# Optimization experiments

Measured on AMD Instinct MI355X. Metric: run time of the kernel, lower is better.

Reference implementation:

```python
import jax, jax.numpy as jnp
import numpy as np

N = 8192
IN_F = 256
HID = 192
OUT_F = 3


def setup_inputs() -> dict:
    key = jax.random.key(0)
    ks = jax.random.split(key, 8)
    features = jax.random.normal(ks[0], (N, IN_F), dtype=jnp.float32)
    # dense (row-stochastic-ish) adjacency; sparse pattern scaled to keep magnitudes sane
    adj = (jax.random.uniform(ks[1], (N, N), dtype=jnp.float32) < (32.0 / N)).astype(jnp.float32) / 32.0
    def winit(k, shape):
        stdv = 0.6 * 6.0 / np.sqrt(shape[0] + shape[1])
        return jax.random.uniform(k, shape, jnp.float32, -stdv, stdv)
    W1 = winit(ks[2], (IN_F, HID))
    b1 = jax.random.uniform(ks[3], (HID,), jnp.float32, -0.1, 0.1)
    W_mid = jnp.stack([winit(jax.random.fold_in(ks[4], i), (HID, HID)) for i in range(12)])
    b_mid = jax.random.uniform(ks[5], (12, HID), jnp.float32, -0.1, 0.1)
    W_out = winit(ks[6], (HID, OUT_F))
    b_out = jax.random.uniform(ks[7], (OUT_F,), jnp.float32, -0.1, 0.1)
    return dict(features=features, adj=adj, W1=W1, b1=b1,
                W_mid=W_mid, b_mid=b_mid, W_out=W_out, b_out=b_out)


def zngcn(x, adj, W, b):
    # support = x @ W; first side_len cols aggregated over adj, rest passed through
    support = x @ W
    side_len = max(W.shape[1] // 3, 2)
    side_1 = adj @ support[:, :side_len]   # [N, side_len]
    out = jnp.concatenate([side_1, support[:, side_len:]], axis=1)
    return out + b


def reference(features, adj, W1, b1, W_mid, b_mid, W_out, b_out):
    relu = jax.nn.relu
    x = relu(zngcn(features, adj, W1, b1))            # gc1
    x = relu(zngcn(x, adj, W_mid[0], b_mid[0]))       # gc2
    feat = (features[:, :HID] + x) * 0.5
    # gc3..gc12 as 5 residual pairs (W_mid indices 1..10)
    for i in (1, 3, 5, 7, 9):
        x = relu(zngcn(feat, adj, W_mid[i], b_mid[i]))
        x = relu(zngcn(x, adj, W_mid[i + 1], b_mid[i + 1]))
        feat = (feat + x) * 0.5
    # gc13 single layer (W_mid index 11)
    x = relu(zngcn(feat, adj, W_mid[11], b_mid[11]))
    feat = (feat + x) * 0.5
    coords = zngcn(feat, adj, W_out, b_out)           # gc14
    return coords, feat
```

## Files before the change

kernel.cpp:

```cpp
#include <hip/hip_runtime.h>
#include <hip/hip_bf16.h>

#define N_NODES 8192
#define CAP 128
#define XSTR 200
#define FFSTR 193
#define NBLK 512
#define SUPSZ (N_NODES * 64)
#define LEAF_BASE 16384

typedef short s16x8 __attribute__((ext_vector_type(8)));
typedef float f32x4 __attribute__((ext_vector_type(4)));
typedef unsigned short u16x8 __attribute__((ext_vector_type(8)));

__device__ __forceinline__ void cstoref(float* p, float v) {
    __hip_atomic_store(p, v, __ATOMIC_RELAXED, __HIP_MEMORY_SCOPE_AGENT);
}
__device__ __forceinline__ void cstoreh(unsigned short* p, unsigned short v) {
    __hip_atomic_store(p, v, __ATOMIC_RELAXED, __HIP_MEMORY_SCOPE_AGENT);
}
__device__ __forceinline__ void cstorei(int* p, int v) {
    __hip_atomic_store(p, v, __ATOMIC_RELAXED, __HIP_MEMORY_SCOPE_AGENT);
}
__device__ __forceinline__ int cloadi(const int* p) {
    return __hip_atomic_load(p, __ATOMIC_RELAXED, __HIP_MEMORY_SCOPE_AGENT);
}
__device__ __forceinline__ float b2f(unsigned short u) {
    union { unsigned int i; float f; } c; c.i = ((unsigned int)u) << 16; return c.f;
}

__global__ __launch_bounds__(256) void prep(
    const unsigned int* __restrict__ adj,
    const float* __restrict__ W1, const float* __restrict__ Wm,
    int* __restrict__ cnt, int* __restrict__ cols,
    unsigned short* __restrict__ Wt1, unsigned short* __restrict__ WtM)
{
    const int tid = threadIdx.x;
    if (blockIdx.x >= 2048) {
        int idx = (int)(blockIdx.x - 2048) * 256 + tid;
        if (idx >= 6144 + 55296) return;
        const float* src; unsigned short* dst; int KT, t, c, lane;
        if (idx < 6144) {
            KT = 8; src = W1; dst = Wt1;
            t = idx / 512; c = (idx >> 6) & 7; lane = idx & 63;
        } else {
            int r = idx - 6144;
            int mat = r / 4608;
            int rem = r % 4608;
            KT = 6; src = Wm + (size_t)mat * 36864; dst = WtM + (size_t)mat * 36864;
            t = rem / 384; c = (rem >> 6) % 6; lane = rem & 63;
        }
        int n = t * 16 + (lane & 15);
        int k0 = c * 32 + ((lane >> 4) << 3);
        u16x8 o;
#pragma unroll
        for (int j = 0; j < 8; ++j)
            o[j] = __bfloat16_as_ushort(__float2bfloat16(src[(size_t)(k0 + j) * 192 + n]));
        *reinterpret_cast<u16x8*>(dst + ((size_t)(t * KT + c) * 64 + lane) * 8) = o;
        return;
    }

    __shared__ int cntL[4];
    __shared__ int colsL[4][CAP];
    const int wave = tid >> 6;
    const int lane = tid & 63;
    const int row = (int)blockIdx.x * 4 + wave;
    if (lane == 0) cntL[wave] = 0;
    __syncthreads();

    const unsigned int* arow = adj + ((size_t)row << 13);
    for (int b = 0; b < 4; ++b) {
        uint4 v[8];
#pragma unroll
        for (int i = 0; i < 8; ++i) {
            int chunk = (b * 8 + i) * 64 + lane;
            v[i] = *reinterpret_cast<const uint4*>(arow + ((size_t)chunk << 2));
        }
#pragma unroll
        for (int i = 0; i < 8; ++i) {
            if ((v[i].x | v[i].y | v[i].z | v[i].w) == 0u) continue;
            int e0 = ((b * 8 + i) * 64 + lane) << 2;
            int loc[4]; int k = 0;
            if (v[i].x) loc[k++] = e0;
            if (v[i].y) loc[k++] = e0 + 1;
            if (v[i].z) loc[k++] = e0 + 2;
            if (v[i].w) loc[k++] = e0 + 3;
            int pos = atomicAdd(&cntL[wave], k);
            for (int j = 0; j < k; ++j)
                if (pos + j < CAP) colsL[wave][pos + j] = loc[j];
        }
    }
    __syncthreads();
    int n = cntL[wave]; if (n > CAP) n = CAP;
    if (lane == 0) cnt[row] = n;
    for (int j = lane; j < CAP; j += 64)
        cols[(size_t)row * CAP + j] = (j < n) ? colsL[wave][j] : 0;
}

__device__ __forceinline__ void gbar_arrive(int* bar, int phase) {
    asm volatile("s_waitcnt vmcnt(0)" ::: "memory");
    __syncthreads();
    if (threadIdx.x == 0)
        cstorei(bar + blockIdx.x * 32, phase);
}
__device__ __forceinline__ void gbar_wait(int* bar, int phase) {
    const int tid = threadIdx.x;
    if (tid < 64) {
        if ((blockIdx.x & 15) == 0) {
            const int leaf = blockIdx.x >> 4;
            int rounds = 0;
            for (;;) {
                int v = (tid < 16) ? cloadi(bar + (leaf * 16 + tid) * 32)
                                   : 0x7fffffff;
#pragma unroll
                for (int off = 32; off > 0; off >>= 1)
                    v = min(v, __shfl_xor(v, off));
                if (v >= phase) break;
                __builtin_amdgcn_s_sleep(1);
                if (++rounds > (1 << 20)) break;
            }
            if (tid == 0) cstorei(bar + LEAF_BASE + leaf * 32, phase);
        }
        int rounds = 0;
        for (;;) {
            int v = (tid < 32) ? cloadi(bar + LEAF_BASE + tid * 32)
                               : 0x7fffffff;
#pragma unroll
            for (int off = 32; off > 0; off >>= 1)
                v = min(v, __shfl_xor(v, off));
            if (v >= phase) break;
            if (rounds < 8) __builtin_amdgcn_s_sleep(1);
            else            __builtin_amdgcn_s_sleep(4);
            if (++rounds > (1 << 20)) break;
        }
    }
    __syncthreads();
}

__device__ __forceinline__ void load_a_feat(s16x8* a, const float* __restrict__ features,
                                            int m0, int lane, int quad) {
    const float* fr = features + (((size_t)(m0 + (lane & 15))) << 8) + quad * 8;
#pragma unroll
    for (int c = 0; c < 8; ++c) {
        float4 f0 = *reinterpret_cast<const float4*>(fr + c * 32);
        float4 f1 = *reinterpret_cast<const float4*>(fr + c * 32 + 4);
        s16x8 v;
        v[0] = (short)__bfloat16_as_ushort(__float2bfloat16(f0.x));
        v[1] = (short)__bfloat16_as_ushort(__float2bfloat16(f0.y));
        v[2] = (short)__bfloat16_as_ushort(__float2bfloat16(f0.z));
        v[3] = (short)__bfloat16_as_ushort(__float2bfloat16(f0.w));
        v[4] = (short)__bfloat16_as_ushort(__float2bfloat16(f1.x));
        v[5] = (short)__bfloat16_as_ushort(__float2bfloat16(f1.y));
        v[6] = (short)__bfloat16_as_ushort(__float2bfloat16(f1.z));
        v[7] = (short)__bfloat16_as_ushort(__float2bfloat16(f1.w));
        a[c] = v;
    }
}

template<int KT, int C0, int C1>
__device__ __forceinline__ void mm_acc(f32x4* acc, const unsigned short* xs,
                                       const unsigned short* __restrict__ Wt,
                                       int lane, int wave, int quad) {
    const short* xr = reinterpret_cast<const short*>(xs) + (lane & 15) * XSTR + quad * 8;
    s16x8 a[C1 - C0];
#pragma unroll
    for (int c = C0; c < C1; ++c)
        a[c - C0] = *reinterpret_cast<const s16x8*>(xr + c * 32);
    const short* wb = reinterpret_cast<const short*>(Wt);
#pragma unroll
    for (int tt = 0; tt < 3; ++tt) {
        const int t = wave * 3 + tt;
        const short* wp = wb + ((size_t)t * KT * 64 + lane) * 8;
#pragma unroll
        for (int c = C0; c < C1; ++c) {
            s16x8 b = *reinterpret_cast<const s16x8*>(wp + (size_t)c * 512);
            acc[tt] = __builtin_amdgcn_mfma_f32_16x16x32_bf16(a[c - C0], b, acc[tt], 0, 0, 0);
        }
    }
}

template<int EP>
__device__ __forceinline__ void mm_epilogue(
    const f32x4* acc, const float* __restrict__ bias,
    unsigned short* __restrict__ supW, unsigned short* xdst, float* featL,
    const float* __restrict__ featG, float* __restrict__ outFeat,
    int m0, int lane, int wave, int quad)
{
#pragma unroll
    for (int tt = 0; tt < 3; ++tt) {
        const int n = (wave * 3 + tt) * 16 + (lane & 15);
#pragma unroll
        for (int r = 0; r < 4; ++r) {
            const int m = quad * 4 + r;
            float v = acc[tt][r];
            if (n < 64) {
                cstoreh(&supW[(((size_t)(m0 + m)) << 6) + n],
                        __bfloat16_as_ushort(__float2bfloat16(v)));
            } else {
                v += bias[n];
                float x = fmaxf(v, 0.f);
                if constexpr (EP == 0) {
                    xdst[m * XSTR + n] = __bfloat16_as_ushort(__float2bfloat16(x));
                } else if constexpr (EP == 1) {
                    float f = (featG[(size_t)(m0 + m) * 256 + n] + x) * 0.5f;
                    featL[m * FFSTR + n] = f;
                    xdst[m * XSTR + n] = __bfloat16_as_ushort(__float2bfloat16(f));
                } else if constexpr (EP == 2) {
                    float f = (featL[m * FFSTR + n] + x) * 0.5f;
                    featL[m * FFSTR + n] = f;
                    xdst[m * XSTR + n] = __bfloat16_as_ushort(__float2bfloat16(f));
                } else {
                    float f = (featL[m * FFSTR + n] + x) * 0.5f;
                    featL[m * FFSTR + n] = f;
                    outFeat[(size_t)(m0 + m) * 192 + n] = f;
                }
            }
        }
    }
}

template<int EP>
__device__ __forceinline__ void agg_phase(
    const unsigned short* __restrict__ supR,
    const int* colsL, const int* cntL,
    const float* __restrict__ bias, unsigned short* xdst,
    float* featL, const float* __restrict__ featG,
    float* __restrict__ outFeat,
    int m0, int lane, int wave)
{
    const int base = wave * 4;
    int na[4];
#pragma unroll
    for (int rr = 0; rr < 4; ++rr) na[rr] = cntL[base + rr];
    int nmax = max(max(na[0], na[1]), max(na[2], na[3]));
    float s[4] = {0.f, 0.f, 0.f, 0.f};
    for (int k = 0; k < nmax; k += 8) {
        float v[32];
#pragma unroll
        for (int rr = 0; rr < 4; ++rr) {
            int4 c0 = *reinterpret_cast<const int4*>(colsL + (base + rr) * CAP + k);
            int4 c1 = *reinterpret_cast<const int4*>(colsL + (base + rr) * CAP + k + 4);
            v[rr * 8 + 0] = b2f(supR[((size_t)(c0.x & 8191) << 6) + lane]);
            v[rr * 8 + 1] = b2f(supR[((size_t)(c0.y & 8191) << 6) + lane]);
            v[rr * 8 + 2] = b2f(supR[((size_t)(c0.z & 8191) << 6) + lane]);
            v[rr * 8 + 3] = b2f(supR[((size_t)(c0.w & 8191) << 6) + lane]);
            v[rr * 8 + 4] = b2f(supR[((size_t)(c1.x & 8191) << 6) + lane]);
            v[rr * 8 + 5] = b2f(supR[((size_t)(c1.y & 8191) << 6) + lane]);
            v[rr * 8 + 6] = b2f(supR[((size_t)(c1.z & 8191) << 6) + lane]);
            v[rr * 8 + 7] = b2f(supR[((size_t)(c1.w & 8191) << 6) + lane]);
        }
#pragma unroll
        for (int rr = 0; rr < 4; ++rr) {
#pragma unroll
            for (int j = 0; j < 8; ++j)
                s[rr] += (k + j < na[rr]) ? v[rr * 8 + j] : 0.f;
        }
    }
#pragma unroll
    for (int rr = 0; rr < 4; ++rr) {
        const int lrow = base + rr;
        const int row = m0 + lrow;
        float vv = s[rr] * 0.03125f + bias[lane];
        float x = fmaxf(vv, 0.f);
        if constexpr (EP == 0) {
            xdst[lrow * XSTR + lane] = __bfloat16_as_ushort(__float2bfloat16(x));
        } else if constexpr (EP == 1) {
            float f = (featG[(size_t)row * 256 + lane] + x) * 0.5f;
            featL[lrow * FFSTR + lane] = f;
            xdst[lrow * XSTR + lane] = __bfloat16_as_ushort(__float2bfloat16(f));
        } else if constexpr (EP == 2) {
            float f = (featL[lrow * FFSTR + lane] + x) * 0.5f;
            featL[lrow * FFSTR + lane] = f;
            xdst[lrow * XSTR + lane] = __bfloat16_as_ushort(__float2bfloat16(f));
        } else {
            float f = (featL[lrow * FFSTR + lane] + x) * 0.5f;
            featL[lrow * FFSTR + lane] = f;
            outFeat[(size_t)row * 192 + lane] = f;
        }
    }
}

template<int EPprev, int EPcur>
__device__ __forceinline__ void layer_step(
    int* bar, int ph,
    unsigned short* xsPrev, unsigned short* xsCur,
    const unsigned short* __restrict__ supPrev, unsigned short* __restrict__ supCur,
    const unsigned short* __restrict__ Wt,
    const float* __restrict__ biasPrev, const float* __restrict__ biasCur,
    float* featL, const float* __restrict__ featG, float* __restrict__ outFeat,
    const int* colsL, const int* cntL,
    int m0, int lane, int wave, int quad)
{
    f32x4 acc[3] = {};
    mm_acc<6, 2, 6>(acc, xsPrev, Wt, lane, wave, quad);
    gbar_wait(bar, ph);
    agg_phase<EPprev>(supPrev, colsL, cntL, biasPrev, xsPrev, featL, featG,
                      outFeat, m0, lane, wave);
    __syncthreads();
    mm_acc<6, 0, 2>(acc, xsPrev, Wt, lane, wave, quad);
    mm_epilogue<EPcur>(acc, biasCur, supCur, xsCur, featL, featG, outFeat,
                       m0, lane, wave, quad);
    gbar_arrive(bar, ph + 1);
}

__global__ __launch_bounds__(256, 2) void fused_layers(
    const float* __restrict__ features,
    const int* __restrict__ cnt, const int* __restrict__ cols,
    const unsigned short* __restrict__ Wt1, const unsigned short* __restrict__ WtM,
    const float* __restrict__ b1, const float* __restrict__ bm,
    const float* __restrict__ Wout, const float* __restrict__ bout,
    unsigned short* __restrict__ supBase, float* __restrict__ sup3,
    float* __restrict__ out, float* __restrict__ outFeat,
    int* __restrict__ bar)
{
    __shared__ unsigned short xsA[16 * XSTR];
    __shared__ unsigned short xsB[16 * XSTR];
    __shared__ float featL[16 * FFSTR];
    __shared__ int colsL[16 * CAP];
    __shared__ int cntL[16];

    const int tid = threadIdx.x;
    const int lane = tid & 63;
    const int wave = tid >> 6;
    const int quad = lane >> 4;
    const int m0 = blockIdx.x * 16;
    int ph = 0;

    for (int i = tid; i < 16 * (CAP / 4); i += 256) {
        int r = i >> 5;
        int g = (i & 31) << 2;
        *reinterpret_cast<int4*>(&colsL[r * CAP + g]) =
            *reinterpret_cast<const int4*>(cols + (size_t)(m0 + r) * CAP + g);
    }
    if (tid < 16) {
        int nn = cnt[m0 + tid];
        cntL[tid] = nn > CAP ? CAP : nn;
    }
    __syncthreads();

    {
        s16x8 a8[8];
        load_a_feat(a8, features, m0, lane, quad);
        f32x4 acc[3] = {};
        const short* wb = reinterpret_cast<const short*>(Wt1);
#pragma unroll
        for (int tt = 0; tt < 3; ++tt) {
            const int t = wave * 3 + tt;
            const short* wp = wb + ((size_t)t * 8 * 64 + lane) * 8;
#pragma unroll
            for (int c = 0; c < 8; ++c) {
                s16x8 b = *reinterpret_cast<const s16x8*>(wp + (size_t)c * 512);
                acc[tt] = __builtin_amdgcn_mfma_f32_16x16x32_bf16(a8[c], b, acc[tt], 0, 0, 0);
            }
        }
        mm_epilogue<0>(acc, b1, supBase, xsA, featL, features, outFeat,
                       m0, lane, wave, quad);
    }
    gbar_arrive(bar, ++ph);

    layer_step<0, 1>(bar, ph, xsA, xsB, supBase, supBase + SUPSZ,
                     WtM, b1, bm, featL, features, outFeat,
                     colsL, cntL, m0, lane, wave, quad);
    ++ph;
    layer_step<1, 0>(bar, ph, xsB, xsA, supBase + SUPSZ, supBase + 2 * SUPSZ,
                     WtM + 36864, bm, bm + 192, featL, features, outFeat,
                     colsL, cntL, m0, lane, wave, quad);
    ++ph;
    layer_step<0, 2>(bar, ph, xsA, xsB, supBase + 2 * SUPSZ, supBase + 3 * SUPSZ,
                     WtM + 2 * 36864, bm + 192, bm + 2 * 192, featL, features,
                     outFeat, colsL, cntL, m0, lane, wave, quad);
    ++ph;

    for (int p = 1; p <= 4; ++p) {
        const int l = 3 + 2 * p;
        layer_step<2, 0>(bar, ph, xsB, xsA,
                         supBase + (size_t)(l - 2) * SUPSZ,
                         supBase + (size_t)(l - 1) * SUPSZ,
                         WtM + (size_t)(l - 2) * 36864,
                         bm + (l - 3) * 192, bm + (l - 2) * 192,
                         featL, features, outFeat, colsL, cntL,
                         m0, lane, wave, quad);
        ++ph;
        const int l2 = l + 1;
        layer_step<0, 2>(bar, ph, xsA, xsB,
                         supBase + (size_t)(l2 - 2) * SUPSZ,
                         supBase + (size_t)(l2 - 1) * SUPSZ,
                         WtM + (size_t)(l2 - 2) * 36864,
                         bm + (l2 - 3) * 192, bm + (l2 - 2) * 192,
                         featL, features, outFeat, colsL, cntL,
                         m0, lane, wave, quad);
        ++ph;
    }

    layer_step<2, 3>(bar, ph, xsB, xsA, supBase + 11 * SUPSZ, supBase + 12 * SUPSZ,
                     WtM + 11 * 36864, bm + 10 * 192, bm + 11 * 192,
                     featL, features, outFeat, colsL, cntL, m0, lane, wave, quad);
    ++ph;

    float s3[4][3];
#pragma unroll
    for (int rr = 0; rr < 4; ++rr) { s3[rr][0] = 0.f; s3[rr][1] = 0.f; s3[rr][2] = 0.f; }
#pragma unroll
    for (int rr = 0; rr < 4; ++rr) {
        const int lrow = wave * 4 + rr;
#pragma unroll
        for (int pp = 1; pp < 3; ++pp) {
            int kk = pp * 64 + lane;
            float f = featL[lrow * FFSTR + kk];
            s3[rr][0] += f * Wout[kk * 3 + 0];
            s3[rr][1] += f * Wout[kk * 3 + 1];
            s3[rr][2] += f * Wout[kk * 3 + 2];
        }
    }
    gbar_wait(bar, ph);
    agg_phase<3>(supBase + (size_t)12 * SUPSZ, colsL, cntL, bm + 11 * 192,
                 xsA, featL, features, outFeat, m0, lane, wave);
    __syncthreads();
#pragma unroll
    for (int rr = 0; rr < 4; ++rr) {
        const int lrow = wave * 4 + rr;
        float f = featL[lrow * FFSTR + lane];
        float s0 = s3[rr][0] + f * Wout[lane * 3 + 0];
        float s1 = s3[rr][1] + f * Wout[lane * 3 + 1];
        float s2 = s3[rr][2] + f * Wout[lane * 3 + 2];
#pragma unroll
        for (int off = 32; off > 0; off >>= 1) {
            s0 += __shfl_down(s0, off);
            s1 += __shfl_down(s1, off);
            s2 += __shfl_down(s2, off);
        }
        if (lane == 0) {
            float* sp = sup3 + (((size_t)(m0 + lrow)) << 2);
            cstoref(sp + 0, s0);
            cstoref(sp + 1, s1);
            cstoref(sp + 2, s2);
        }
    }
    gbar_arrive(bar, ++ph);
    gbar_wait(bar, ph);

    {
        const int lrow = tid >> 4;
        const int row = m0 + lrow;
        const int sub = tid & 15;
        int n = cntL[lrow];
        const int* cl = colsL + lrow * CAP;
        float s0 = 0.f, s1 = 0.f;
        for (int k = sub; k < n; k += 16) {
            int j = cl[k];
            s0 += sup3[((size_t)j << 2) + 0];
            s1 += sup3[((size_t)j << 2) + 1];
        }
#pragma unroll
        for (int off = 8; off > 0; off >>= 1) {
            s0 += __shfl_down(s0, off, 16);
            s1 += __shfl_down(s1, off, 16);
        }
        if (sub == 0) {
            float* op = out + (size_t)row * 3;
            op[0] = s0 * 0.03125f + bout[0];
            op[1] = s1 * 0.03125f + bout[1];
            op[2] = sup3[((size_t)row << 2) + 2] + bout[2];
        }
    }
}

extern "C" void kernel_launch(void* const* d_in, const int* in_sizes, int n_in,
                              void* d_out, int out_size, void* d_ws, size_t ws_size,
                              hipStream_t stream) {
    const float* features = (const float*)d_in[0];
    const unsigned int* adj = (const unsigned int*)d_in[1];
    const float* W1 = (const float*)d_in[2];
    const float* b1 = (const float*)d_in[3];
    const float* Wm = (const float*)d_in[4];
    const float* bm = (const float*)d_in[5];
    const float* Wo = (const float*)d_in[6];
    const float* bo = (const float*)d_in[7];
    float* out = (float*)d_out;
    float* outFeat = out + (size_t)N_NODES * 3;

    char* w = (char*)d_ws;
    int* bar = (int*)(w);
    int* cnt = (int*)(w + 131072);
    int* cols = (int*)(w + 163840);
    unsigned short* supBase = (unsigned short*)(w + 4358144);
    float* sup3 = (float*)(w + 17989632);
    unsigned short* Wt1 = (unsigned short*)(w + 18120704);
    unsigned short* WtM = (unsigned short*)(w + 18219008);

    hipMemsetAsync(bar, 0, 131072, stream);
    prep<<<2288, 256, 0, stream>>>(adj, W1, Wm, cnt, cols, Wt1, WtM);
    fused_layers<<<NBLK, 256, 0, stream>>>(features, cnt, cols, Wt1, WtM, b1, bm,
                                           Wo, bo, supBase, sup3, out, outFeat, bar);

    (void)in_sizes; (void)n_in; (void)out_size; (void)ws_size;
}
```

Measured before the change: 562.2 us.

## Compute aggregated support columns first and arrive at barrier before pass-through columns

Each layer's GEMM is reordered so every wave first computes the 64 aggregated support columns (one 16-col tile per wave), stores them, and signals the grid barrier before computing the remaining 128 pass-through columns and their epilogue. This moves barrier arrival earlier so other blocks can begin aggregation sooner, overlapping the pass-through work with barrier latency. The earlier pre-barrier partial-K GEMM overlap is removed, and the layer-1 GEMM now runs before the column-list loads. The prep kernel also double-buffers adjacency row loads.

```diff
diff --git a/kernel.cpp b/kernel.cpp
--- a/kernel.cpp
+++ b/kernel.cpp
@@ -27,6 +27,9 @@
 }
 __device__ __forceinline__ float b2f(unsigned short u) {
     union { unsigned int i; float f; } c; c.i = ((unsigned int)u) << 16; return c.f;
+}
+__device__ __forceinline__ unsigned short f2b(float f) {
+    return __bfloat16_as_ushort(__float2bfloat16(f));
 }
 
 __global__ __launch_bounds__(256) void prep(
@@ -55,7 +58,7 @@
         u16x8 o;
 #pragma unroll
         for (int j = 0; j < 8; ++j)
-            o[j] = __bfloat16_as_ushort(__float2bfloat16(src[(size_t)(k0 + j) * 192 + n]));
+            o[j] = f2b(src[(size_t)(k0 + j) * 192 + n]);
         *reinterpret_cast<u16x8*>(dst + ((size_t)(t * KT + c) * 64 + lane) * 8) = o;
         return;
     }
@@ -69,13 +72,18 @@
     __syncthreads();
 
     const unsigned int* arow = adj + ((size_t)row << 13);
-    for (int b = 0; b < 4; ++b) {
-        uint4 v[8];
+    uint4 buf[2][8];
+    auto loadb = [&](int b, uint4* v) {
 #pragma unroll
         for (int i = 0; i < 8; ++i) {
             int chunk = (b * 8 + i) * 64 + lane;
             v[i] = *reinterpret_cast<const uint4*>(arow + ((size_t)chunk << 2));
         }
+    };
+    loadb(0, buf[0]);
+    for (int b = 0; b < 4; ++b) {
+        if (b < 3) loadb(b + 1, buf[(b + 1) & 1]);
+        uint4* v = buf[b & 1];
 #pragma unroll
         for (int i = 0; i < 8; ++i) {
             if ((v[i].x | v[i].y | v[i].z | v[i].w) == 0u) continue;
@@ -137,6 +145,14 @@
     __syncthreads();
 }
 
+template<int KT>
+__device__ __forceinline__ void load_a(s16x8* a, const unsigned short* xs,
+                                       int lane, int quad) {
+    const short* xr = reinterpret_cast<const short*>(xs) + (lane & 15) * XSTR + quad * 8;
+#pragma unroll
+    for (int c = 0; c < KT; ++c) a[c] = *reinterpret_cast<const s16x8*>(xr + c * 32);
+}
+
 __device__ __forceinline__ void load_a_feat(s16x8* a, const float* __restrict__ features,
                                             int m0, int lane, int quad) {
     const float* fr = features + (((size_t)(m0 + (lane & 15))) << 8) + quad * 8;
@@ -145,76 +161,40 @@
         float4 f0 = *reinterpret_cast<const float4*>(fr + c * 32);
         float4 f1 = *reinterpret_cast<const float4*>(fr + c * 32 + 4);
         s16x8 v;
-        v[0] = (short)__bfloat16_as_ushort(__float2bfloat16(f0.x));
-        v[1] = (short)__bfloat16_as_ushort(__float2bfloat16(f0.y));
-        v[2] = (short)__bfloat16_as_ushort(__float2bfloat16(f0.z));
-        v[3] = (short)__bfloat16_as_ushort(__float2bfloat16(f0.w));
-        v[4] = (short)__bfloat16_as_ushort(__float2bfloat16(f1.x));
-        v[5] = (short)__bfloat16_as_ushort(__float2bfloat16(f1.y));
-        v[6] = (short)__bfloat16_as_ushort(__float2bfloat16(f1.z));
-        v[7] = (short)__bfloat16_as_ushort(__float2bfloat16(f1.w));
+        v[0] = (short)f2b(f0.x); v[1] = (short)f2b(f0.y);
+        v[2] = (short)f2b(f0.z); v[3] = (short)f2b(f0.w);
+        v[4] = (short)f2b(f1.x); v[5] = (short)f2b(f1.y);
+        v[6] = (short)f2b(f1.z); v[7] = (short)f2b(f1.w);
         a[c] = v;
     }
 }
 
-template<int KT, int C0, int C1>
-__device__ __forceinline__ void mm_acc(f32x4* acc, const unsigned short* xs,
-                                       const unsigned short* __restrict__ Wt,
-                                       int lane, int wave, int quad) {
-    const short* xr = reinterpret_cast<const short*>(xs) + (lane & 15) * XSTR + quad * 8;
-    s16x8 a[C1 - C0];
-#pragma unroll
-    for (int c = C0; c < C1; ++c)
-        a[c - C0] = *reinterpret_cast<const s16x8*>(xr + c * 32);
-    const short* wb = reinterpret_cast<const short*>(Wt);
-#pragma unroll
-    for (int tt = 0; tt < 3; ++tt) {
-        const int t = wave * 3 + tt;
-        const short* wp = wb + ((size_t)t * KT * 64 + lane) * 8;
-#pragma unroll
-        for (int c = C0; c < C1; ++c) {
-            s16x8 b = *reinterpret_cast<const s16x8*>(wp + (size_t)c * 512);
-            acc[tt] = __builtin_amdgcn_mfma_f32_16x16x32_bf16(a[c - C0], b, acc[tt], 0, 0, 0);
-        }
-    }
-}
-
 template<int EP>
-__device__ __forceinline__ void mm_epilogue(
-    const f32x4* acc, const float* __restrict__ bias,
-    unsigned short* __restrict__ supW, unsigned short* xdst, float* featL,
+__device__ __forceinline__ void pass_epilogue(
+    const f32x4& acc, int n, const float* __restrict__ bias,
+    unsigned short* xdst, float* featL,
     const float* __restrict__ featG, float* __restrict__ outFeat,
-    int m0, int lane, int wave, int quad)
+    int m0, int quad)
 {
 #pragma unroll
-    for (int tt = 0; tt < 3; ++tt) {
-        const int n = (wave * 3 + tt) * 16 + (lane & 15);
-#pragma unroll
-        for (int r = 0; r < 4; ++r) {
-            const int m = quad * 4 + r;
-            float v = acc[tt][r];
-            if (n < 64) {
-                cstoreh(&supW[(((size_t)(m0 + m)) << 6) + n],
-                        __bfloat16_as_ushort(__float2bfloat16(v)));
-            } else {
-                v += bias[n];
-                float x = fmaxf(v, 0.f);
-                if constexpr (EP == 0) {
-                    xdst[m * XSTR + n] = __bfloat16_as_ushort(__float2bfloat16(x));
-                } else if constexpr (EP == 1) {
-                    float f = (featG[(size_t)(m0 + m) * 256 + n] + x) * 0.5f;
-                    featL[m * FFSTR + n] = f;
-                    xdst[m * XSTR + n] = __bfloat16_as_ushort(__float2bfloat16(f));
-                } else if constexpr (EP == 2) {
-                    float f = (featL[m * FFSTR + n] + x) * 0.5f;
-                    featL[m * FFSTR + n] = f;
-                    xdst[m * XSTR + n] = __bfloat16_as_ushort(__float2bfloat16(f));
-                } else {
-                    float f = (featL[m * FFSTR + n] + x) * 0.5f;
-                    featL[m * FFSTR + n] = f;
-                    outFeat[(size_t)(m0 + m) * 192 + n] = f;
-                }
-            }
+    for (int r = 0; r < 4; ++r) {
+        const int m = quad * 4 + r;
+        float v = acc[r] + bias[n];
+        float x = fmaxf(v, 0.f);
+        if constexpr (EP == 0) {
+            xdst[m * XSTR + n] = f2b(x);
+        } else if constexpr (EP == 1) {
+            float f = (featG[(size_t)(m0 + m) * 256 + n] + x) * 0.5f;
+            featL[m * FFSTR + n] = f;
+            xdst[m * XSTR + n] = f2b(f);
+        } else if constexpr (EP == 2) {
+            float f = (featL[m * FFSTR + n] + x) * 0.5f;
+            featL[m * FFSTR + n] = f;
+            xdst[m * XSTR + n] = f2b(f);
+        } else {
+            float f = (featL[m * FFSTR + n] + x) * 0.5f;
+            featL[m * FFSTR + n] = f;
+            outFeat[(size_t)(m0 + m) * 192 + n] = f;
         }
     }
 }
@@ -263,15 +243,15 @@
         float vv = s[rr] * 0.03125f + bias[lane];
         float x = fmaxf(vv, 0.f);
         if constexpr (EP == 0) {
-            xdst[lrow * XSTR + lane] = __bfloat16_as_ushort(__float2bfloat16(x));
+            xdst[lrow * XSTR + lane] = f2b(x);
         } else if constexpr (EP == 1) {
             float f = (featG[(size_t)row * 256 + lane] + x) * 0.5f;
             featL[lrow * FFSTR + lane] = f;
-            xdst[lrow * XSTR + lane] = __bfloat16_as_ushort(__float2bfloat16(f));
+            xdst[lrow * XSTR + lane] = f2b(f);
         } else if constexpr (EP == 2) {
             float f = (featL[lrow * FFSTR + lane] + x) * 0.5f;
             featL[lrow * FFSTR + lane] = f;
-            xdst[lrow * XSTR + lane] = __bfloat16_as_ushort(__float2bfloat16(f));
+            xdst[lrow * XSTR + lane] = f2b(f);
         } else {
             float f = (featL[lrow * FFSTR + lane] + x) * 0.5f;
             featL[lrow * FFSTR + lane] = f;
@@ -291,16 +271,40 @@
     const int* colsL, const int* cntL,
     int m0, int lane, int wave, int quad)
 {
-    f32x4 acc[3] = {};
-    mm_acc<6, 2, 6>(acc, xsPrev, Wt, lane, wave, quad);
     gbar_wait(bar, ph);
     agg_phase<EPprev>(supPrev, colsL, cntL, biasPrev, xsPrev, featL, featG,
                       outFeat, m0, lane, wave);
     __syncthreads();
-    mm_acc<6, 0, 2>(acc, xsPrev, Wt, lane, wave, quad);
-    mm_epilogue<EPcur>(acc, biasCur, supCur, xsCur, featL, featG, outFeat,
-                       m0, lane, wave, quad);
+    s16x8 a[6];
+    load_a<6>(a, xsPrev, lane, quad);
+    const short* wb = reinterpret_cast<const short*>(Wt);
+    {
+        f32x4 accS = {};
+        const short* wp = wb + ((size_t)wave * 6 * 64 + lane) * 8;
+#pragma unroll
+        for (int c = 0; c < 6; ++c) {
+            s16x8 b = *reinterpret_cast<const s16x8*>(wp + (size_t)c * 512);
+            accS = __builtin_amdgcn_mfma_f32_16x16x32_bf16(a[c], b, accS, 0, 0, 0);
+        }
+        const int n = wave * 16 + (lane & 15);
+#pragma unroll
+        for (int r = 0; r < 4; ++r)
+            cstoreh(&supCur[(((size_t)(m0 + quad * 4 + r)) << 6) + n], f2b(accS[r]));
+    }
     gbar_arrive(bar, ph + 1);
+#pragma unroll
+    for (int p = 0; p < 2; ++p) {
+        const int t = 4 + p * 4 + wave;
+        f32x4 acc = {};
+        const short* wp = wb + ((size_t)t * 6 * 64 + lane) * 8;
+#pragma unroll
+        for (int c = 0; c < 6; ++c) {
+            s16x8 b = *reinterpret_cast<const s16x8*>(wp + (size_t)c * 512);
+            acc = __builtin_amdgcn_mfma_f32_16x16x32_bf16(a[c], b, acc, 0, 0, 0);
+        }
+        const int n = t * 16 + (lane & 15);
+        pass_epilogue<EPcur>(acc, n, biasCur, xsCur, featL, featG, outFeat, m0, quad);
+    }
 }
 
 __global__ __launch_bounds__(256, 2) void fused_layers(
@@ -324,8 +328,39 @@
     const int wave = tid >> 6;
     const int quad = lane >> 4;
     const int m0 = blockIdx.x * 16;
-    int ph = 0;
-
+
+    {
+        s16x8 a8[8];
+        load_a_feat(a8, features, m0, lane, quad);
+        const short* wb = reinterpret_cast<const short*>(Wt1);
+        {
+            f32x4 accS = {};
+            const short* wp = wb + ((size_t)wave * 8 * 64 + lane) * 8;
+#pragma unroll
+            for (int c = 0; c < 8; ++c) {
+                s16x8 b = *reinterpret_cast<const s16x8*>(wp + (size_t)c * 512);
+                accS = __builtin_amdgcn_mfma_f32_16x16x32_bf16(a8[c], b, accS, 0, 0, 0);
+            }
+            const int n = wave * 16 + (lane & 15);
+#pragma unroll
+            for (int r = 0; r < 4; ++r)
+                cstoreh(&supBase[(((size_t)(m0 + quad * 4 + r)) << 6) + n], f2b(accS[r]));
+        }
+        gbar_arrive(bar, 1);
+#pragma unroll
+        for (int p = 0; p < 2; ++p) {
+            const int t = 4 + p * 4 + wave;
+            f32x4 acc = {};
+            const short* wp = wb + ((size_t)t * 8 * 64 + lane) * 8;
+#pragma unroll
+            for (int c = 0; c < 8; ++c) {
+                s16x8 b = *reinterpret_cast<const s16x8*>(wp + (size_t)c * 512);
+                acc = __builtin_amdgcn_mfma_f32_16x16x32_bf16(a8[c], b, acc, 0, 0, 0);
+            }
+            const int n = t * 16 + (lane & 15);
+            pass_epilogue<0>(acc, n, b1, xsA, featL, features, outFeat, m0, quad);
+        }
+    }
     for (int i = tid; i < 16 * (CAP / 4); i += 256) {
         int r = i >> 5;
         int g = (i & 31) << 2;
@@ -336,28 +371,8 @@
         int nn = cnt[m0 + tid];
         cntL[tid] = nn > CAP ? CAP : nn;
     }
-    __syncthreads();
-
-    {
-        s16x8 a8[8];
-        load_a_feat(a8, features, m0, lane, quad);
-        f32x4 acc[3] = {};
-        const short* wb = reinterpret_cast<const short*>(Wt1);
-#pragma unroll
-        for (int tt = 0; tt < 3; ++tt) {
-            const int t = wave * 3 + tt;
-            const short* wp = wb + ((size_t)t * 8 * 64 + lane) * 8;
-#pragma unroll
-            for (int c = 0; c < 8; ++c) {
-                s16x8 b = *reinterpret_cast<const s16x8*>(wp + (size_t)c * 512);
-                acc[tt] = __builtin_amdgcn_mfma_f32_16x16x32_bf16(a8[c], b, acc[tt], 0, 0, 0);
-            }
-        }
-        mm_epilogue<0>(acc, b1, supBase, xsA, featL, features, outFeat,
-                       m0, lane, wave, quad);
-    }
-    gbar_arrive(bar, ++ph);
-
+
+    int ph = 1;
     layer_step<0, 1>(bar, ph, xsA, xsB, supBase, supBase + SUPSZ,
                      WtM, b1, bm, featL, features, outFeat,
                      colsL, cntL, m0, lane, wave, quad);
@@ -397,6 +412,7 @@
                      featL, features, outFeat, colsL, cntL, m0, lane, wave, quad);
     ++ph;
 
+    __syncthreads();
     float s3[4][3];
 #pragma unroll
     for (int rr = 0; rr < 4; ++rr) { s3[rr][0] = 0.f; s3[rr][1] = 0.f; s3[rr][2] = 0.f; }
```

Result: slower. 585.5 us (+4.1%).
